# Kernel tuning notes

Measured on AMD Instinct MI355X. Metric: run time of the kernel, lower is better.

The kernel has to match this reference:

```python
import jax, jax.numpy as jnp
import numpy as np

N_NODES = 100000
N_EDGES = 3200000
N_FEAT = 128
N_HID = 64


def gcn_conv(x, src, dst, ew, W, b, n):
    # x: [N, Fin]; src/dst: [E'] incl. self-loops; ew: [E'] edge weights
    xw = x @ W  # [N, Fout]
    deg = jax.ops.segment_sum(ew, dst, num_segments=n)  # [N]
    dinv = jnp.where(deg > 0, jax.lax.rsqrt(jnp.maximum(deg, 1e-12)), 0.0)
    norm = dinv[src] * ew * dinv[dst]  # [E']
    out = jax.ops.segment_sum(norm[:, None] * xw[src], dst, num_segments=n)
    return out + b


def setup_inputs() -> dict:
    key = jax.random.key(0)
    k = jax.random.split(key, 8)
    x = jax.random.normal(k[0], (N_NODES, N_FEAT), dtype=jnp.float32)
    edge_index = jax.random.randint(k[1], (2, N_EDGES), 0, N_NODES, dtype=jnp.int32)
    edge_attr = jax.random.uniform(k[2], (N_EDGES,), dtype=jnp.float32)
    s1 = 1.0 / np.sqrt(N_FEAT)
    s2 = 1.0 / np.sqrt(N_HID)
    W1 = jax.random.uniform(k[3], (N_FEAT, N_HID), minval=-s1, maxval=s1, dtype=jnp.float32)
    b1 = jnp.zeros((N_HID,), dtype=jnp.float32)
    W2 = jax.random.uniform(k[4], (N_HID, 1), minval=-s2, maxval=s2, dtype=jnp.float32)
    b2 = jnp.zeros((1,), dtype=jnp.float32)
    return {"x": x, "edge_index": edge_index, "edge_attr": edge_attr,
            "W1": W1, "b1": b1, "W2": W2, "b2": b2}


def reference(x, edge_index, edge_attr, W1, b1, W2, b2):
    n = x.shape[0]
    # add self-loops with weight 1 (PyG gcn_norm, improved=False)
    loop = jnp.arange(n, dtype=edge_index.dtype)
    src = jnp.concatenate([edge_index[0], loop])
    dst = jnp.concatenate([edge_index[1], loop])
    ew = jnp.concatenate([edge_attr, jnp.ones((n,), dtype=edge_attr.dtype)])
    h = gcn_conv(x, src, dst, ew, W1, b1, n)
    h = jax.nn.relu(h)
    # dropout is identity in eval mode
    out = gcn_conv(h, src, dst, ew, W2, b2, n)
    return out
```

## Files before the change

### kernel.cpp

```cpp
#include <hip/hip_runtime.h>
#include <hip/hip_fp16.h>


#define NPB_LOG 9
#define NPB     512
#define PCAP    17408
#define NEDG    8192

typedef _Float16 f16x8 __attribute__((ext_vector_type(8)));
typedef float    f32x4 __attribute__((ext_vector_type(4)));

__global__ void k_initcur(int* __restrict__ gcur, int npart) {
    int i = blockIdx.x * blockDim.x + threadIdx.x;
    if (i < npart) gcur[i] = i * PCAP;
}

__global__ __launch_bounds__(256) void k_binA(const int* __restrict__ src,
                                              const int* __restrict__ dst,
                                              const float* __restrict__ ea,
                                              int* __restrict__ gcur,
                                              uint2* __restrict__ part,
                                              int E, int npart) {
    __shared__ uint2 stag[NEDG];
    __shared__ unsigned char stagb[NEDG];
    __shared__ int hist[256];
    __shared__ int lofs[256];
    __shared__ int base[256];
    int t = threadIdx.x;
    int c0 = blockIdx.x * NEDG;
    hist[t] = 0;
    __syncthreads();
    for (int j = t; j < NEDG; j += 256) {
        int e = c0 + j;
        if (e < E) atomicAdd(&hist[dst[e] >> NPB_LOG], 1);
    }
    __syncthreads();
    int v = hist[t];
    lofs[t] = v;
    __syncthreads();
    for (int off = 1; off < 256; off <<= 1) {
        int u = (t >= off) ? lofs[t - off] : 0;
        __syncthreads();
        lofs[t] += u;
        __syncthreads();
    }
    int excl = lofs[t] - v;
    if (t < npart && v > 0) base[t] = atomicAdd(&gcur[t], v);
    __syncthreads();
    lofs[t] = excl;
    hist[t] = excl;
    __syncthreads();
    for (int j = t; j < NEDG; j += 256) {
        int e = c0 + j;
        if (e < E) {
            int d = dst[e];
            int b = d >> NPB_LOG;
            int p = atomicAdd(&hist[b], 1);
            stag[p]  = make_uint2((uint)src[e] | ((uint)(d & (NPB - 1)) << 17),
                                  __float_as_uint(ea[e]));
            stagb[p] = (unsigned char)b;
        }
    }
    __syncthreads();
    int nvalid = min(NEDG, E - c0);
    for (int j = t; j < nvalid; j += 256) {
        int b = stagb[j];
        int gp = base[b] + (j - lofs[b]);
        if (gp < (b + 1) * PCAP) part[gp] = stag[j];
    }
}

__global__ __launch_bounds__(512) void k_binB(const int* __restrict__ gcur,
                                              const uint2* __restrict__ part,
                                              int2* __restrict__ ecsr,
                                              int* __restrict__ rowstart,
                                              int* __restrict__ cntg,
                                              float* __restrict__ dinv, int n) {
    __shared__ int   cnt[NPB];
    __shared__ float wsum[NPB];
    __shared__ int   cur[NPB];
    __shared__ int   wsums[8];
    int b = blockIdx.x;
    int t = threadIdx.x;
    int lane = t & 63, wv = t >> 6;
    cnt[t] = 0; wsum[t] = 0.0f;
    __syncthreads();
    int beg = b * PCAP;
    int len = gcur[b] - beg;
    if (len > PCAP) len = PCAP;
    for (int j = t; j < len; j += NPB) {
        uint2 ed = part[beg + j];
        int dlow = (ed.x >> 17) & (NPB - 1);
        atomicAdd(&cnt[dlow], 1);
        atomicAdd(&wsum[dlow], __uint_as_float(ed.y));
    }
    __syncthreads();
    int v = cnt[t];
    int s = v;
    for (int off = 1; off < 64; off <<= 1) {
        int u = __shfl_up(s, off, 64);
        if (lane >= off) s += u;
    }
    if (lane == 63) wsums[wv] = s;
    __syncthreads();
    if (t < 64) {
        int x = (t < 8) ? wsums[t] : 0;
        for (int off = 1; off < 8; off <<= 1) {
            int u = __shfl_up(x, off, 64);
            if (lane >= off) x += u;
        }
        if (t < 8) wsums[t] = x;
    }
    __syncthreads();
    int excl = s - v + (wv > 0 ? wsums[wv - 1] : 0);
    cur[t] = excl;
    int node = (b << NPB_LOG) + t;
    if (node < n) {
        rowstart[node] = beg + excl;
        cntg[node]     = v;
        dinv[node]     = rsqrtf(1.0f + wsum[t]);
    }
    __syncthreads();
    for (int j = t; j < len; j += NPB) {
        uint2 ed = part[beg + j];
        int dlow = (ed.x >> 17) & (NPB - 1);
        int p = atomicAdd(&cur[dlow], 1);
        ecsr[beg + p] = make_int2((int)(ed.x & 0x1FFFF), (int)ed.y);
    }
}

#define XPAD 136
__global__ __launch_bounds__(256) void k_gemm1m(const float* __restrict__ x,
                                                const float* __restrict__ W1,
                                                const float* __restrict__ dinv,
                                                __half* __restrict__ xw2, int n) {
    __shared__ __align__(16) _Float16 xs[64 * XPAD];
    __shared__ __align__(16) _Float16 wt[64 * XPAD];
    int tid = threadIdx.x;
    int row0 = blockIdx.x * 64;
    for (int i = tid; i < 64 * 32; i += 256) {
        int r = i >> 5, k4 = i & 31;
        float4 f = make_float4(0.f, 0.f, 0.f, 0.f);
        int gr = row0 + r;
        if (gr < n) f = ((const float4*)x)[(size_t)gr * 32 + k4];
        union { _Float16 h[4]; uint2 u; } tmp;
        tmp.h[0] = (_Float16)f.x; tmp.h[1] = (_Float16)f.y;
        tmp.h[2] = (_Float16)f.z; tmp.h[3] = (_Float16)f.w;
        *(uint2*)&xs[r * XPAD + k4 * 4] = tmp.u;
    }
    for (int i = tid; i < 128 * 64; i += 256) {
        int k = i >> 6, nn = i & 63;
        wt[nn * XPAD + k] = (_Float16)W1[i];
    }
    __syncthreads();

    int strip = tid >> 6;
    int lane  = tid & 63;
    int quad  = lane >> 4;
    int m     = lane & 15;
    f32x4 acc[4] = {{0,0,0,0},{0,0,0,0},{0,0,0,0},{0,0,0,0}};
#pragma unroll
    for (int kc = 0; kc < 4; ++kc) {
        f16x8 a = *(const f16x8*)&xs[(strip * 16 + m) * XPAD + kc * 32 + quad * 8];
#pragma unroll
        for (int nt = 0; nt < 4; ++nt) {
            f16x8 b = *(const f16x8*)&wt[(nt * 16 + m) * XPAD + kc * 32 + quad * 8];
            acc[nt] = __builtin_amdgcn_mfma_f32_16x16x32_f16(a, b, acc[nt], 0, 0, 0);
        }
    }
    float dv[4];
#pragma unroll
    for (int reg = 0; reg < 4; ++reg) {
        int gr = row0 + strip * 16 + quad * 4 + reg;
        dv[reg] = (gr < n) ? dinv[gr] : 0.0f;
    }
#pragma unroll
    for (int nt = 0; nt < 4; ++nt) {
#pragma unroll
        for (int reg = 0; reg < 4; ++reg) {
            int gr = row0 + strip * 16 + quad * 4 + reg;
            if (gr < n)
                xw2[(size_t)gr * 64 + nt * 16 + m] = __float2half(dv[reg] * acc[nt][reg]);
        }
    }
}

__global__ __launch_bounds__(256) void k_agg1f(const int* __restrict__ rowstart,
                                               const int* __restrict__ cntg,
                                               const int2* __restrict__ ecsr,
                                               const float* __restrict__ dinv,
                                               const __half* __restrict__ xw2,
                                               const float* __restrict__ b1,
                                               const float* __restrict__ W2,
                                               float* __restrict__ g, int n) {
    int i = blockIdx.x * 4 + (threadIdx.x >> 6);
    int lane = threadIdx.x & 63;
    if (i >= n) return;
    int beg = __builtin_amdgcn_readfirstlane(rowstart[i]);
    int len = __builtin_amdgcn_readfirstlane(cntg[i]);
    const int2* __restrict__ ep = ecsr + beg;

    float a0 = __half2float(xw2[(size_t)i * 64 + lane]);
    float a1 = 0.0f, a2 = 0.0f, a3 = 0.0f;
    int j = 0;
    for (; j + 8 <= len; j += 8) {
        int2 e0 = ep[j + 0];
        int2 e1 = ep[j + 1];
        int2 e2 = ep[j + 2];
        int2 e3 = ep[j + 3];
        int2 e4 = ep[j + 4];
        int2 e5 = ep[j + 5];
        int2 e6 = ep[j + 6];
        int2 e7 = ep[j + 7];
        float v0 = __half2float(xw2[(size_t)e0.x * 64 + lane]);
        float v1 = __half2float(xw2[(size_t)e1.x * 64 + lane]);
        float v2 = __half2float(xw2[(size_t)e2.x * 64 + lane]);
        float v3 = __half2float(xw2[(size_t)e3.x * 64 + lane]);
        float v4 = __half2float(xw2[(size_t)e4.x * 64 + lane]);
        float v5 = __half2float(xw2[(size_t)e5.x * 64 + lane]);
        float v6 = __half2float(xw2[(size_t)e6.x * 64 + lane]);
        float v7 = __half2float(xw2[(size_t)e7.x * 64 + lane]);
        a0 += __int_as_float(e0.y) * v0;
        a1 += __int_as_float(e1.y) * v1;
        a2 += __int_as_float(e2.y) * v2;
        a3 += __int_as_float(e3.y) * v3;
        a0 += __int_as_float(e4.y) * v4;
        a1 += __int_as_float(e5.y) * v5;
        a2 += __int_as_float(e6.y) * v6;
        a3 += __int_as_float(e7.y) * v7;
    }
    for (; j < len; ++j) {
        int2 e = ep[j];
        a0 += __int_as_float(e.y) * __half2float(xw2[(size_t)e.x * 64 + lane]);
    }
    float acc = (a0 + a1) + (a2 + a3);
    float di = dinv[i];
    float h = fmaxf(di * acc + b1[lane], 0.0f) * W2[lane];
    for (int off = 32; off; off >>= 1) h += __shfl_down(h, off, 64);
    if (lane == 0) g[i] = di * h;
}

__global__ __launch_bounds__(256) void k_agg2(const int* __restrict__ rowstart,
                                              const int* __restrict__ cntg,
                                              const int2* __restrict__ ecsr,
                                              const float* __restrict__ dinv,
                                              const float* __restrict__ g,
                                              const float* __restrict__ b2,
                                              float* __restrict__ out, int n) {
    int i = blockIdx.x * 4 + (threadIdx.x >> 6);
    int lane = threadIdx.x & 63;
    if (i >= n) return;
    size_t beg = (size_t)rowstart[i];
    int len = cntg[i];
    float p = 0.0f;
    for (int j = lane; j < len; j += 64) {
        int2 ed = ecsr[beg + j];
        p += __int_as_float(ed.y) * g[ed.x];
    }
    for (int off = 32; off; off >>= 1) p += __shfl_down(p, off, 64);
    if (lane == 0) out[i] = b2[0] + dinv[i] * (g[i] + p);
}

extern "C" void kernel_launch(void* const* d_in, const int* in_sizes, int n_in,
                              void* d_out, int out_size, void* d_ws, size_t ws_size,
                              hipStream_t stream) {
    const float* x  = (const float*)d_in[0];
    const int*   ei = (const int*)  d_in[1];
    const float* ea = (const float*)d_in[2];
    const float* W1 = (const float*)d_in[3];
    const float* b1 = (const float*)d_in[4];
    const float* W2 = (const float*)d_in[5];
    const float* b2 = (const float*)d_in[6];
    float* out = (float*)d_out;

    int n = in_sizes[0] / 128;
    int E = in_sizes[1] / 2;
    const int* src = ei;
    const int* dst = ei + E;
    int npart = (n + NPB - 1) >> NPB_LOG;

    int*    ws       = (int*)d_ws;
    int*    gcur     = ws;
    uint2*  part     = (uint2*)(ws + 256);
    __half* xw2      = (__half*)part;
    size_t  psz      = (size_t)npart * PCAP;
    int2*   ecsr     = (int2*)(ws + 256 + psz * 2);
    int*    rowstart = ws + 256 + psz * 4;
    int*    cntg     = rowstart + n;
    float*  dinv     = (float*)(cntg + n);
    float*  g        = dinv + n;

    k_initcur<<<1, 256, 0, stream>>>(gcur, npart);
    k_binA  <<<(E + NEDG - 1) / NEDG, 256, 0, stream>>>(src, dst, ea, gcur, part, E, npart);
    k_binB  <<<npart, NPB, 0, stream>>>(gcur, part, ecsr, rowstart, cntg, dinv, n);
    k_gemm1m<<<(n + 63) / 64, 256, 0, stream>>>(x, W1, dinv, xw2, n);
    k_agg1f <<<(n + 3) / 4, 256, 0, stream>>>(rowstart, cntg, ecsr, dinv, xw2, b1, W2, g, n);
    k_agg2  <<<(n + 3) / 4, 256, 0, stream>>>(rowstart, cntg, ecsr, dinv, g, b2, out, n);
}
```

Measured before the change: 329.2 us.

## Halve partition size to 256 nodes, widen binning histogram, pack row descriptors

Node partitions for binning shrink from 512 to 256 nodes, and edge chunks per block shrink from 8192 to 4096. The first binning pass therefore handles up to 512 buckets, with a two-per-thread scan and 16-bit bucket tags. The aim is to run more, smaller second-pass blocks, each with 256 threads and less shared memory, for better occupancy and parallelism. Row start and count are packed into one int2 descriptor, so the aggregation kernels make a single load per node, and agg2 now uses readfirstlane. The risks are more global atomics on partition cursors and more scattered partition writes.

```diff
diff --git a/kernel.cpp b/kernel.cpp
--- a/kernel.cpp
+++ b/kernel.cpp
@@ -2,10 +2,10 @@
 #include <hip/hip_fp16.h>
 
 
-#define NPB_LOG 9
-#define NPB     512
-#define PCAP    17408
-#define NEDG    8192
+#define NPB_LOG 8
+#define NPB     256
+#define PCAP    8832
+#define NEDG    4096
 
 typedef _Float16 f16x8 __attribute__((ext_vector_type(8)));
 typedef float    f32x4 __attribute__((ext_vector_type(4)));
@@ -22,33 +22,40 @@
                                               uint2* __restrict__ part,
                                               int E, int npart) {
     __shared__ uint2 stag[NEDG];
-    __shared__ unsigned char stagb[NEDG];
-    __shared__ int hist[256];
-    __shared__ int lofs[256];
-    __shared__ int base[256];
+    __shared__ unsigned short stagb[NEDG];
+    __shared__ int hist[512];
+    __shared__ int lofs[512];
+    __shared__ int base[512];
+    __shared__ int tsum[256];
     int t = threadIdx.x;
     int c0 = blockIdx.x * NEDG;
-    hist[t] = 0;
+    hist[t] = 0; hist[t + 256] = 0;
     __syncthreads();
     for (int j = t; j < NEDG; j += 256) {
         int e = c0 + j;
         if (e < E) atomicAdd(&hist[dst[e] >> NPB_LOG], 1);
     }
     __syncthreads();
-    int v = hist[t];
-    lofs[t] = v;
+    int h0 = hist[2 * t], h1 = hist[2 * t + 1];
+    int s = h0 + h1;
+    tsum[t] = s;
     __syncthreads();
     for (int off = 1; off < 256; off <<= 1) {
-        int u = (t >= off) ? lofs[t - off] : 0;
+        int u = (t >= off) ? tsum[t - off] : 0;
         __syncthreads();
-        lofs[t] += u;
+        tsum[t] += u;
         __syncthreads();
     }
-    int excl = lofs[t] - v;
-    if (t < npart && v > 0) base[t] = atomicAdd(&gcur[t], v);
-    __syncthreads();
-    lofs[t] = excl;
-    hist[t] = excl;
+    int texcl = tsum[t] - s;
+    lofs[2 * t]     = texcl;
+    lofs[2 * t + 1] = texcl + h0;
+    __syncthreads();
+    for (int b = t; b < npart; b += 256) {
+        int v = hist[b];
+        if (v > 0) base[b] = atomicAdd(&gcur[b], v);
+    }
+    __syncthreads();
+    for (int b = t; b < 512; b += 256) hist[b] = lofs[b];
     __syncthreads();
     for (int j = t; j < NEDG; j += 256) {
         int e = c0 + j;
@@ -58,7 +65,7 @@
             int p = atomicAdd(&hist[b], 1);
             stag[p]  = make_uint2((uint)src[e] | ((uint)(d & (NPB - 1)) << 17),
                                   __float_as_uint(ea[e]));
-            stagb[p] = (unsigned char)b;
+            stagb[p] = (unsigned short)b;
         }
     }
     __syncthreads();
@@ -70,16 +77,15 @@
     }
 }
 
-__global__ __launch_bounds__(512) void k_binB(const int* __restrict__ gcur,
+__global__ __launch_bounds__(256) void k_binB(const int* __restrict__ gcur,
                                               const uint2* __restrict__ part,
                                               int2* __restrict__ ecsr,
-                                              int* __restrict__ rowstart,
-                                              int* __restrict__ cntg,
+                                              int2* __restrict__ rowdesc,
                                               float* __restrict__ dinv, int n) {
     __shared__ int   cnt[NPB];
     __shared__ float wsum[NPB];
     __shared__ int   cur[NPB];
-    __shared__ int   wsums[8];
+    __shared__ int   wsums[4];
     int b = blockIdx.x;
     int t = threadIdx.x;
     int lane = t & 63, wv = t >> 6;
@@ -103,22 +109,14 @@
     }
     if (lane == 63) wsums[wv] = s;
     __syncthreads();
-    if (t < 64) {
-        int x = (t < 8) ? wsums[t] : 0;
-        for (int off = 1; off < 8; off <<= 1) {
-            int u = __shfl_up(x, off, 64);
-            if (lane >= off) x += u;
-        }
-        if (t < 8) wsums[t] = x;
-    }
-    __syncthreads();
-    int excl = s - v + (wv > 0 ? wsums[wv - 1] : 0);
+    int wbase = 0;
+    for (int k = 0; k < wv; ++k) wbase += wsums[k];
+    int excl = s - v + wbase;
     cur[t] = excl;
     int node = (b << NPB_LOG) + t;
     if (node < n) {
-        rowstart[node] = beg + excl;
-        cntg[node]     = v;
-        dinv[node]     = rsqrtf(1.0f + wsum[t]);
+        rowdesc[node] = make_int2(beg + excl, v);
+        dinv[node]    = rsqrtf(1.0f + wsum[t]);
     }
     __syncthreads();
     for (int j = t; j < len; j += NPB) {
@@ -185,8 +183,7 @@
     }
 }
 
-__global__ __launch_bounds__(256) void k_agg1f(const int* __restrict__ rowstart,
-                                               const int* __restrict__ cntg,
+__global__ __launch_bounds__(256) void k_agg1f(const int2* __restrict__ rowdesc,
                                                const int2* __restrict__ ecsr,
                                                const float* __restrict__ dinv,
                                                const __half* __restrict__ xw2,
@@ -196,8 +193,9 @@
     int i = blockIdx.x * 4 + (threadIdx.x >> 6);
     int lane = threadIdx.x & 63;
     if (i >= n) return;
-    int beg = __builtin_amdgcn_readfirstlane(rowstart[i]);
-    int len = __builtin_amdgcn_readfirstlane(cntg[i]);
+    int2 rd = rowdesc[i];
+    int beg = __builtin_amdgcn_readfirstlane(rd.x);
+    int len = __builtin_amdgcn_readfirstlane(rd.y);
     const int2* __restrict__ ep = ecsr + beg;
 
     float a0 = __half2float(xw2[(size_t)i * 64 + lane]);
@@ -212,14 +210,14 @@
         int2 e5 = ep[j + 5];
         int2 e6 = ep[j + 6];
         int2 e7 = ep[j + 7];
-        float v0 = __half2float(xw2[(size_t)e0.x * 64 + lane]);
-        float v1 = __half2float(xw2[(size_t)e1.x * 64 + lane]);
-        float v2 = __half2float(xw2[(size_t)e2.x * 64 + lane]);
-        float v3 = __half2float(xw2[(size_t)e3.x * 64 + lane]);
-        float v4 = __half2float(xw2[(size_t)e4.x * 64 + lane]);
-        float v5 = __half2float(xw2[(size_t)e5.x * 64 + lane]);
-        float v6 = __half2float(xw2[(size_t)e6.x * 64 + lane]);
-        float v7 = __half2float(xw2[(size_t)e7.x * 64 + lane]);
+        float v0 = __half2float(xw2[(size_t)(uint)e0.x * 64 + lane]);
+        float v1 = __half2float(xw2[(size_t)(uint)e1.x * 64 + lane]);
+        float v2 = __half2float(xw2[(size_t)(uint)e2.x * 64 + lane]);
+        float v3 = __half2float(xw2[(size_t)(uint)e3.x * 64 + lane]);
+        float v4 = __half2float(xw2[(size_t)(uint)e4.x * 64 + lane]);
+        float v5 = __half2float(xw2[(size_t)(uint)e5.x * 64 + lane]);
+        float v6 = __half2float(xw2[(size_t)(uint)e6.x * 64 + lane]);
+        float v7 = __half2float(xw2[(size_t)(uint)e7.x * 64 + lane]);
         a0 += __int_as_float(e0.y) * v0;
         a1 += __int_as_float(e1.y) * v1;
         a2 += __int_as_float(e2.y) * v2;
@@ -231,7 +229,7 @@
     }
     for (; j < len; ++j) {
         int2 e = ep[j];
-        a0 += __int_as_float(e.y) * __half2float(xw2[(size_t)e.x * 64 + lane]);
+        a0 += __int_as_float(e.y) * __half2float(xw2[(size_t)(uint)e.x * 64 + lane]);
     }
     float acc = (a0 + a1) + (a2 + a3);
     float di = dinv[i];
@@ -240,8 +238,7 @@
     if (lane == 0) g[i] = di * h;
 }
 
-__global__ __launch_bounds__(256) void k_agg2(const int* __restrict__ rowstart,
-                                              const int* __restrict__ cntg,
+__global__ __launch_bounds__(256) void k_agg2(const int2* __restrict__ rowdesc,
                                               const int2* __restrict__ ecsr,
                                               const float* __restrict__ dinv,
                                               const float* __restrict__ g,
@@ -250,11 +247,13 @@
     int i = blockIdx.x * 4 + (threadIdx.x >> 6);
     int lane = threadIdx.x & 63;
     if (i >= n) return;
-    size_t beg = (size_t)rowstart[i];
-    int len = cntg[i];
+    int2 rd = rowdesc[i];
+    int beg = __builtin_amdgcn_readfirstlane(rd.x);
+    int len = __builtin_amdgcn_readfirstlane(rd.y);
+    const int2* __restrict__ ep = ecsr + beg;
     float p = 0.0f;
     for (int j = lane; j < len; j += 64) {
-        int2 ed = ecsr[beg + j];
+        int2 ed = ep[j];
         p += __int_as_float(ed.y) * g[ed.x];
     }
     for (int off = 32; off; off >>= 1) p += __shfl_down(p, off, 64);
@@ -281,19 +280,18 @@
 
     int*    ws       = (int*)d_ws;
     int*    gcur     = ws;
-    uint2*  part     = (uint2*)(ws + 256);
+    uint2*  part     = (uint2*)(ws + 512);
     __half* xw2      = (__half*)part;
     size_t  psz      = (size_t)npart * PCAP;
-    int2*   ecsr     = (int2*)(ws + 256 + psz * 2);
-    int*    rowstart = ws + 256 + psz * 4;
-    int*    cntg     = rowstart + n;
-    float*  dinv     = (float*)(cntg + n);
+    int2*   ecsr     = (int2*)(ws + 512 + psz * 2);
+    int2*   rowdesc  = (int2*)(ws + 512 + psz * 4);
+    float*  dinv     = (float*)(ws + 512 + psz * 4 + (size_t)2 * n);
     float*  g        = dinv + n;
 
-    k_initcur<<<1, 256, 0, stream>>>(gcur, npart);
+    k_initcur<<<(npart + 255) / 256, 256, 0, stream>>>(gcur, npart);
     k_binA  <<<(E + NEDG - 1) / NEDG, 256, 0, stream>>>(src, dst, ea, gcur, part, E, npart);
-    k_binB  <<<npart, NPB, 0, stream>>>(gcur, part, ecsr, rowstart, cntg, dinv, n);
+    k_binB  <<<npart, NPB, 0, stream>>>(gcur, part, ecsr, rowdesc, dinv, n);
     k_gemm1m<<<(n + 63) / 64, 256, 0, stream>>>(x, W1, dinv, xw2, n);
-    k_agg1f <<<(n + 3) / 4, 256, 0, stream>>>(rowstart, cntg, ecsr, dinv, xw2, b1, W2, g, n);
-    k_agg2  <<<(n + 3) / 4, 256, 0, stream>>>(rowstart, cntg, ecsr, dinv, g, b2, out, n);
-}
+    k_agg1f <<<(n + 3) / 4, 256, 0, stream>>>(rowdesc, ecsr, dinv, xw2, b1, W2, g, n);
+    k_agg2  <<<(n + 3) / 4, 256, 0, stream>>>(rowdesc, ecsr, dinv, g, b2, out, n);
+}
```

Result: slower. 335.8 us (+2.0%).
